# Performance work log

Hardware: AMD Instinct MI355X
Metric: run time of the kernel (lower is better)

Reference implementation:

```python
import jax, jax.numpy as jnp
import numpy as np

FEAT = 1433
HID = 2
NUM_CLASS = 7
EPS = 1e-5  # torch BatchNorm1d default eps


def _bn_softsign(h, gamma, beta):
    # BatchNorm1d in training mode: batch stats over (batch, length) per channel.
    mu = h.mean(axis=(0, 2), keepdims=True)
    var = h.var(axis=(0, 2), keepdims=True)  # biased, matches torch normalization
    hn = (h - mu) * jax.lax.rsqrt(var + EPS)
    hn = hn * gamma[None, :, None] + beta[None, :, None]
    return hn / (1.0 + jnp.abs(hn))  # Softsign


def feature_adjacency(x, y):
    # (x.unsqueeze(-1) * y.unsqueeze(-2)).sum(dim=1) with x channel dim == 1
    # reduces to an outer product of x[:,0] with neighbor.sum over K.
    adj = jnp.einsum('bf,bg->bfg', x.sum(1), y.sum(1))  # [B,F,F]
    adj = adj + jnp.swapaxes(adj, -1, -2)
    adj = jnp.sqrt(adj)
    # row_normalize: divide by sum over dim 1, zero out inf/nan
    norm = adj / adj.sum(axis=1, keepdims=True)
    norm = jnp.where(jnp.isfinite(norm), norm, 0.0)
    return norm + jnp.eye(FEAT, dtype=x.dtype)


def featbrd(x, adj, W, b):
    # adjacency-based feature conv: y[b,c,f] = sum_g adj[(b),f,g] x[b,c,g],
    # then 1x1 conv over channels (Conv1d kernel_size=1).
    if adj.shape[0] == 1:
        y = jnp.einsum('fg,bcg->bcf', adj[0], x)
    else:
        y = jnp.einsum('bfg,bcg->bcf', adj, x)
    return jnp.einsum('oc,bcf->bof', W, y) + b[None, :, None]


def setup_inputs() -> dict:
    key = jax.random.key(0)
    ks = jax.random.split(key, 10)
    B, K = 64, 8
    inp = {
        'x': jax.random.uniform(ks[0], (B, 1, FEAT), dtype=jnp.float32),
        'neighbor': jax.random.uniform(ks[1], (B, K, FEAT), dtype=jnp.float32),
        'adj_buf': jnp.zeros((1, FEAT, FEAT), jnp.float32),
        'W1': jax.random.normal(ks[2], (HID, 1), jnp.float32) * 0.5,
        'b1': jnp.zeros((HID,), jnp.float32),
        'W2': jax.random.normal(ks[3], (HID, HID), jnp.float32) * 0.5,
        'b2': jnp.zeros((HID,), jnp.float32),
        'g1': jnp.ones((HID,), jnp.float32),
        'be1': jnp.zeros((HID,), jnp.float32),
        'g2': jnp.ones((HID,), jnp.float32),
        'be2': jnp.zeros((HID,), jnp.float32),
        'Wc': jax.random.normal(ks[4], (NUM_CLASS, FEAT * HID), jnp.float32) * 0.02,
        'bc': jnp.zeros((NUM_CLASS,), jnp.float32),
    }
    return inp


def reference(x, neighbor, adj_buf, W1, b1, W2, b2, g1, be1, g2, be2, Wc, bc):
    fadj = feature_adjacency(x, neighbor)          # [B,F,F]
    adj_tot = adj_buf + fadj.sum(0)                # [1,F,F] (buffer starts at zero)
    h = _bn_softsign(featbrd(x, fadj, W1, b1), g1, be1)      # [B,HID,F]
    h = _bn_softsign(featbrd(h, adj_tot, W2, b2), g2, be2)   # [B,HID,F]
    flat = h.reshape(h.shape[0], -1)               # Flatten (C then F, row-major)
    return flat @ Wc.T + bc
```

## Files before the change

kernel.cpp:

```cpp
#include <hip/hip_runtime.h>
#include <hip/hip_bf16.h>
#include <math.h>

constexpr int F   = 1433;
constexpr int NB  = 64;
constexpr int KN  = 8;
constexpr int BF  = NB * F;
constexpr float EPS = 1e-5f;

constexpr int SF  = 16;
constexpr int CH  = 90;
constexpr int AbS = 1440;
constexpr int SK  = 15;
constexpr int FT  = 12;
constexpr int NA  = 720;
constexpr int NST = 256;

constexpr int O_YS  = 0;
constexpr int O_DP  = O_YS + BF;
constexpr int O_Y1P = O_DP + SF * BF;
constexpr int O_P   = O_Y1P + SF * BF;
constexpr int O_Y1  = O_P + 4 * BF;
constexpr int O_Y2  = O_Y1 + BF;
constexpr int O_G2P = O_Y2 + 2 * BF;
constexpr int O_AB  = O_G2P + SK * 128 * F;
constexpr int O_ST  = O_AB + (F * AbS) / 2;
constexpr int O_BAR = O_ST + 64;

__device__ __forceinline__ void devst(float* p, float v) {
  __hip_atomic_store(p, v, __ATOMIC_RELAXED, __HIP_MEMORY_SCOPE_AGENT);
}
__device__ __forceinline__ void devst16(ushort* p, ushort v) {
  __hip_atomic_store(p, v, __ATOMIC_RELAXED, __HIP_MEMORY_SCOPE_AGENT);
}
__device__ __forceinline__ void devst4(float4* p, float4 v) {
  union { float2 f; unsigned long long u; } lo, hi;
  lo.f = make_float2(v.x, v.y);
  hi.f = make_float2(v.z, v.w);
  unsigned long long* q = (unsigned long long*)p;
  __hip_atomic_store(q + 0, lo.u, __ATOMIC_RELAXED, __HIP_MEMORY_SCOPE_AGENT);
  __hip_atomic_store(q + 1, hi.u, __ATOMIC_RELAXED, __HIP_MEMORY_SCOPE_AGENT);
}
__device__ __forceinline__ float devld(const float* p) {
  return __hip_atomic_load(p, __ATOMIC_RELAXED, __HIP_MEMORY_SCOPE_AGENT);
}

__device__ __forceinline__ void grid_barrier(unsigned* bar, unsigned phase) {
  __syncthreads();
  if (threadIdx.x == 0) {
    const unsigned ngrp = gridDim.x >> 3;
    const unsigned grp = (unsigned)blockIdx.x & 7u;
    unsigned old = __hip_atomic_fetch_add(&bar[grp * 32], 1u,
                                          __ATOMIC_RELAXED, __HIP_MEMORY_SCOPE_AGENT);
    if (old == phase * ngrp - 1u) {
      unsigned m = __hip_atomic_fetch_add(&bar[256], 1u,
                                          __ATOMIC_RELAXED, __HIP_MEMORY_SCOPE_AGENT);
      if (m == phase * 8u - 1u)
        __hip_atomic_store(&bar[257], phase, __ATOMIC_RELAXED, __HIP_MEMORY_SCOPE_AGENT);
    }
    while (__hip_atomic_load(&bar[257], __ATOMIC_RELAXED, __HIP_MEMORY_SCOPE_AGENT) < phase)
      __builtin_amdgcn_s_sleep(32);
  }
  __syncthreads();
}

__global__ __launch_bounds__(256, 4) void k_fused(
    const float* __restrict__ x, const float* __restrict__ nbr,
    const float* __restrict__ W1, const float* __restrict__ g1,
    const float* __restrict__ be1, const float* __restrict__ W2,
    const float* __restrict__ b2, const float* __restrict__ g2,
    const float* __restrict__ be2, const float* __restrict__ Wc,
    const float* __restrict__ bc, float* __restrict__ out,
    float* __restrict__ ws) {
  float*  ys  = ws + O_YS;
  float*  DP  = ws + O_DP;
  float*  Y1P = ws + O_Y1P;
  float4* P   = (float4*)(ws + O_P);
  float*  y1  = ws + O_Y1;
  float*  y2  = ws + O_Y2;
  float*  G2P = ws + O_G2P;
  ushort* Ab  = (ushort*)(ws + O_AB);
  const ushort* Abu = (const ushort*)(ws + O_AB);
  float*  st  = ws + O_ST;
  unsigned* bar = (unsigned*)(ws + O_BAR);

  __shared__ __align__(16) char smem[21504];
  const int tid = threadIdx.x;
  const int gsz = (int)gridDim.x;

  {
    float2* xyc = (float2*)smem;
    for (int w = blockIdx.x; w < NB * SF; w += gsz) {
      const int b = w & 63, s = w >> 6;
      __syncthreads();
      const int cs = s * CH, cn = min(CH, F - cs);
      for (int i = tid; i < cn; i += 256) {
        const float* p = nbr + (size_t)b * KN * F + cs + i;
        float a = 0.f;
#pragma unroll
        for (int k = 0; k < KN; ++k) a += p[k * F];
        xyc[i] = make_float2(x[b * F + cs + i], a);
      }
      __syncthreads();
      float gx[6], gy[6], acc[6] = {};
#pragma unroll
      for (int j = 0; j < 6; ++j) {
        int g = tid + 256 * j;
        int gc = min(g, F - 1);
        const float* p = nbr + (size_t)b * KN * F + gc;
        float a = 0.f;
#pragma unroll
        for (int k = 0; k < KN; ++k) a += p[k * F];
        gx[j] = (g < F) ? x[b * F + gc] : 0.f;
        gy[j] = (g < F) ? a : 0.f;
      }
      if (s == 0) {
#pragma unroll
        for (int j = 0; j < 6; ++j) {
          int g = tid + 256 * j;
          if (g < F) devst(&ys[b * F + g], gy[j]);
        }
      }
#pragma unroll 6
      for (int i = 0; i < cn; ++i) {
        float2 p = xyc[i];
#pragma unroll
        for (int j = 0; j < 6; ++j)
          acc[j] += __builtin_amdgcn_sqrtf(fmaf(gy[j], p.x, gx[j] * p.y));
      }
#pragma unroll
      for (int j = 0; j < 6; ++j) {
        int g = tid + 256 * j;
        if (g < F) devst(&DP[(size_t)s * BF + b * F + g], acc[j]);
      }
    }
  }
  grid_barrier(bar, 1u);

  {
    float4* pl = (float4*)smem;
    for (int w = blockIdx.x; w < NB * SF; w += gsz) {
      const int b = w & 63, s = w >> 6;
      __syncthreads();
      const int cs = s * CH, cn = min(CH, F - cs);
      for (int i = tid; i < cn; i += 256) {
        int g = cs + i;
        float d = 0.f;
#pragma unroll
        for (int t = 0; t < SF; ++t) d += DP[(size_t)t * BF + b * F + g];
        float inv = (d > 0.f) ? 1.f / d : 0.f;
        float xv = x[b * F + g], yv = ys[b * F + g];
        float4 pv = make_float4(xv, yv, xv * inv, inv);
        pl[i] = pv;
        devst4(&P[b * F + g], pv);
      }
      __syncthreads();
      float fx[6], fys[6], acc[6] = {};
#pragma unroll
      for (int j = 0; j < 6; ++j) {
        int f = tid + 256 * j;
        fx[j]  = (f < F) ? x[b * F + f] : 0.f;
        fys[j] = (f < F) ? ys[b * F + f] : 0.f;
      }
#pragma unroll 6
      for (int i = 0; i < cn; ++i) {
        float4 p = pl[i];
#pragma unroll
        for (int j = 0; j < 6; ++j)
          acc[j] = fmaf(__builtin_amdgcn_sqrtf(fmaf(fx[j], p.y, fys[j] * p.x)), p.z, acc[j]);
      }
#pragma unroll
      for (int j = 0; j < 6; ++j) {
        int f = tid + 256 * j;
        if (f < F) devst(&Y1P[(size_t)s * BF + b * F + f], acc[j]);
      }
    }
  }
  grid_barrier(bar, 2u);

  {
    for (int w = blockIdx.x; w < NA + NST; w += gsz) {
      __syncthreads();
      if (w < NA) {
        float2 (*fxy)[NB] = (float2(*)[NB])smem;
        const int gxc = w % 6, fyt = w / 6;
        const int fbase = fyt * FT;
#pragma unroll
        for (int r = 0; r < 3; ++r) {
          int i = tid + 256 * r;
          int j = i >> 6, bb = i & 63;
          int f = fbase + j;
          float vx = 0.f, vy = 0.f;
          if (f < F) { vx = x[bb * F + f]; vy = ys[bb * F + f]; }
          fxy[j][bb] = make_float2(vx, vy);
        }
        __syncthreads();
        const int g = gxc * 256 + tid;
        if (g < F) {
          float acc[FT] = {};
          float4 cur[4], nxt[4];
#pragma unroll
          for (int t = 0; t < 4; ++t) cur[t] = P[t * F + g];
          for (int bb = 0; bb < NB; bb += 4) {
            if (bb + 4 < NB) {
#pragma unroll
              for (int t = 0; t < 4; ++t) nxt[t] = P[(bb + 4 + t) * F + g];
            }
#pragma unroll
            for (int t = 0; t < 4; ++t) {
              float4 pc = cur[t];
#pragma unroll
              for (int j = 0; j < FT; ++j) {
                float2 wv = fxy[j][bb + t];
                acc[j] = fmaf(__builtin_amdgcn_sqrtf(fmaf(wv.x, pc.y, pc.x * wv.y)), pc.w, acc[j]);
              }
            }
#pragma unroll
            for (int t = 0; t < 4; ++t) cur[t] = nxt[t];
          }
#pragma unroll
          for (int j = 0; j < FT; ++j) {
            int f = fbase + j;
            if (f < F) {
              __hip_bfloat16 hv = __float2bfloat16(acc[j]);
              devst16(&Ab[(size_t)f * AbS + g], *reinterpret_cast<ushort*>(&hv));
            }
          }
        } else if (g < AbS) {
#pragma unroll
          for (int j = 0; j < FT; ++j) {
            int f = fbase + j;
            if (f < F) devst16(&Ab[(size_t)f * AbS + g], (ushort)0);
          }
        }
      } else {
        const int sid = w - NA;
        float sv = 0.f, sq = 0.f;
        for (int i = sid * 256 + tid; i < BF; i += NST * 256) {
          float v = x[i];
#pragma unroll
          for (int t = 0; t < SF; ++t) v += Y1P[(size_t)t * BF + i];
          devst(&y1[i], v);
          sv += v; sq += v * v;
        }
#pragma unroll
        for (int o = 32; o; o >>= 1) {
          sv += __shfl_down(sv, o, 64);
          sq += __shfl_down(sq, o, 64);
        }
        float* ls = (float*)smem;
        float* lq = ls + 4;
        int wave = tid >> 6, lane = tid & 63;
        if (lane == 0) { ls[wave] = sv; lq[wave] = sq; }
        __syncthreads();
        if (tid == 0) {
          atomicAdd(&st[0], ls[0] + ls[1] + ls[2] + ls[3]);
          atomicAdd(&st[1], lq[0] + lq[1] + lq[2] + lq[3]);
        }
      }
    }
  }
  grid_barrier(bar, 3u);

  {
    const float mu  = st[0] / (float)BF;
    const float var = st[1] / (float)BF - mu * mu;
    const float wa = W1[0], wb = W1[1];
    const float k0 = wa * g1[0] / sqrtf(wa * wa * var + EPS);
    const float k1 = wb * g1[1] / sqrtf(wb * wb * var + EPS);
    const float c0 = -k0 * mu + be1[0];
    const float c1 = -k1 * mu + be1[1];

    float* Al = (float*)smem;
    float* Hl = (float*)(smem + 4608);
    const int ffs = tid >> 3, g4s = (tid & 7) * 4;
    const int hb = tid & 7, hg = tid >> 3;
    const int fsub = (tid & 7) * 4, msub = (tid >> 3) * 4;

    for (int w = blockIdx.x; w < 45 * SK; w += gsz) {
      const int fb = w % 45, sk = w / 45;
      const int f0 = fb * 32;
      const int gs = sk * 96;
      __syncthreads();

      uint2 pa; float pyv[8];
      auto loadRegs = [&](int gb) {
        const int f = f0 + ffs;
        pa = make_uint2(0u, 0u);
        if (f < F) pa = *(const uint2*)&Abu[(size_t)f * AbS + gb + g4s];
        const int gl = min(gb + hg, F - 1);
#pragma unroll
        for (int r = 0; r < 8; ++r) pyv[r] = y1[(hb + 8 * r) * F + gl];
      };
      auto storeLDS = [&]() {
        Al[(g4s + 0) * 36 + ffs] = __uint_as_float(pa.x << 16);
        Al[(g4s + 1) * 36 + ffs] = __uint_as_float(pa.x & 0xffff0000u);
        Al[(g4s + 2) * 36 + ffs] = __uint_as_float(pa.y << 16);
        Al[(g4s + 3) * 36 + ffs] = __uint_as_float(pa.y & 0xffff0000u);
#pragma unroll
        for (int r = 0; r < 8; ++r) {
          const int bb = hb + 8 * r;
          const float v = pyv[r];
          float h0 = fmaf(k0, v, c0); h0 = h0 / (1.f + fabsf(h0));
          float h1 = fmaf(k1, v, c1); h1 = h1 / (1.f + fabsf(h1));
          *(float2*)&Hl[hg * 132 + 2 * bb] = make_float2(h0, h1);
        }
      };

      float acc[4][4] = {};
      loadRegs(gs);
      for (int c = 0; c < 3; ++c) {
        if (c) __syncthreads();
        storeLDS();
        __syncthreads();
        if (c < 2) loadRegs(gs + (c + 1) * 32);
#pragma unroll 4
        for (int gi = 0; gi < 32; ++gi) {
          float4 a4 = *(const float4*)&Al[gi * 36 + fsub];
          float4 h4 = *(const float4*)&Hl[gi * 132 + msub];
          float av[4] = {a4.x, a4.y, a4.z, a4.w};
          float hv[4] = {h4.x, h4.y, h4.z, h4.w};
#pragma unroll
          for (int i = 0; i < 4; ++i)
#pragma unroll
            for (int j = 0; j < 4; ++j)
              acc[i][j] = fmaf(av[i], hv[j], acc[i][j]);
        }
      }
      float* dst = G2P + (size_t)sk * 128 * F;
#pragma unroll
      for (int i = 0; i < 4; ++i) {
        int f = f0 + fsub + i;
        if (f < F) {
#pragma unroll
          for (int j = 0; j < 4; ++j)
            devst(&dst[(msub + j) * F + f], acc[i][j]);
        }
      }
    }
  }
  grid_barrier(bar, 4u);

  {
    const float mu  = st[0] / (float)BF;
    const float var = st[1] / (float)BF - mu * mu;
    const float wa = W1[0], wb = W1[1];
    const float k0 = wa * g1[0] / sqrtf(wa * wa * var + EPS);
    const float k1 = wb * g1[1] / sqrtf(wb * wb * var + EPS);
    const float c0 = -k0 * mu + be1[0];
    const float c1 = -k1 * mu + be1[1];

    float su = 0.f, sv = 0.f, suu = 0.f, svv = 0.f, suv = 0.f;
    for (int i = blockIdx.x * 256 + tid; i < BF; i += gsz * 256) {
      int b = i / F, f = i - b * F;
      float wv = y1[i];
      float h0 = fmaf(k0, wv, c0); h0 = h0 / (1.f + fabsf(h0));
      float h1 = fmaf(k1, wv, c1); h1 = h1 / (1.f + fabsf(h1));
      int iu = (2 * b) * F + f, iv = iu + F;
      float u = 64.f * h0, v = 64.f * h1;
#pragma unroll
      for (int t = 0; t < SK; ++t) {
        u += G2P[(size_t)t * 128 * F + iu];
        v += G2P[(size_t)t * 128 * F + iv];
      }
      devst(&y2[iu], u); devst(&y2[iv], v);
      su += u; sv += v; suu += u * u; svv += v * v; suv += u * v;
    }
#pragma unroll
    for (int o = 32; o; o >>= 1) {
      su  += __shfl_down(su, o, 64);
      sv  += __shfl_down(sv, o, 64);
      suu += __shfl_down(suu, o, 64);
      svv += __shfl_down(svv, o, 64);
      suv += __shfl_down(suv, o, 64);
    }
    float (*red)[4] = (float(*)[4])smem;
    int wave = tid >> 6, lane = tid & 63;
    if (lane == 0) {
      red[0][wave] = su; red[1][wave] = sv; red[2][wave] = suu;
      red[3][wave] = svv; red[4][wave] = suv;
    }
    __syncthreads();
    if (tid == 0) {
#pragma unroll
      for (int m = 0; m < 5; ++m)
        atomicAdd(&st[2 + m], red[m][0] + red[m][1] + red[m][2] + red[m][3]);
    }
  }
  grid_barrier(bar, 5u);

  {
    float n = (float)BF;
    float Eu = devld(&st[2]) / n, Ev = devld(&st[3]) / n;
    float Euu = devld(&st[4]) / n, Evv = devld(&st[5]) / n, Euv = devld(&st[6]) / n;
    float cA[2], cB[2], cC[2];
#pragma unroll
    for (int o = 0; o < 2; ++o) {
      float w0 = W2[o * 2 + 0], w1 = W2[o * 2 + 1];
      float mean = w0 * Eu + w1 * Ev + b2[o];
      float Eh2 = w0 * w0 * Euu + 2.f * w0 * w1 * Euv + w1 * w1 * Evv +
                  2.f * b2[o] * (w0 * Eu + w1 * Ev) + b2[o] * b2[o];
      float vr = Eh2 - mean * mean;
      float inv = g2[o] / sqrtf(vr + EPS);
      cA[o] = w0 * inv;
      cB[o] = w1 * inv;
      cC[o] = (b2[o] - mean) * inv + be2[o];
    }
    float (*red)[4] = (float(*)[4])smem;
    for (int w = blockIdx.x; w < NB * 6; w += gsz) {
      const int b = w / 6, part = w % 6;
      float acc[7] = {};
      const int f = part * 256 + tid;
      if (f < F) {
        float u = y2[(2 * b) * F + f], v = y2[(2 * b + 1) * F + f];
        float h0 = fmaf(cA[0], u, fmaf(cB[0], v, cC[0]));
        h0 = h0 / (1.f + fabsf(h0));
        float h1 = fmaf(cA[1], u, fmaf(cB[1], v, cC[1]));
        h1 = h1 / (1.f + fabsf(h1));
#pragma unroll
        for (int o = 0; o < 7; ++o)
          acc[o] = fmaf(Wc[o * (2 * F) + f], h0, Wc[o * (2 * F) + F + f] * h1);
      }
#pragma unroll
      for (int o = 0; o < 7; ++o) {
#pragma unroll
        for (int s2 = 32; s2; s2 >>= 1) acc[o] += __shfl_down(acc[o], s2, 64);
      }
      __syncthreads();
      int wave = tid >> 6, lane = tid & 63;
      if (lane == 0) {
#pragma unroll
        for (int o = 0; o < 7; ++o) red[o][wave] = acc[o];
      }
      __syncthreads();
      if (tid < 7) {
        float add = red[tid][0] + red[tid][1] + red[tid][2] + red[tid][3];
        if (part == 0) add += bc[tid];
        atomicAdd(&out[b * 7 + tid], add);
      }
    }
  }
}

__global__ __launch_bounds__(256) void k_D(const float* __restrict__ x,
                                           const float* __restrict__ nbr,
                                           float* __restrict__ DP,
                                           float* __restrict__ ys_out,
                                           float* __restrict__ st) {
  const int b = blockIdx.x, s = blockIdx.y;
  if (b == 0 && s == 0 && threadIdx.x < 64) st[threadIdx.x] = 0.f;
  __shared__ __align__(8) float2 xyc[CH];
  const int cs = s * CH, cn = min(CH, F - cs);
  for (int i = threadIdx.x; i < cn; i += 256) {
    const float* p = nbr + (size_t)b * KN * F + cs + i;
    float a = 0.f;
#pragma unroll
    for (int k = 0; k < KN; ++k) a += p[k * F];
    xyc[i] = make_float2(x[b * F + cs + i], a);
  }
  __syncthreads();
  float gx[6], gy[6], acc[6] = {};
#pragma unroll
  for (int j = 0; j < 6; ++j) {
    int g = threadIdx.x + 256 * j;
    int gc = min(g, F - 1);
    const float* p = nbr + (size_t)b * KN * F + gc;
    float a = 0.f;
#pragma unroll
    for (int k = 0; k < KN; ++k) a += p[k * F];
    gx[j] = (g < F) ? x[b * F + gc] : 0.f;
    gy[j] = (g < F) ? a : 0.f;
  }
  if (s == 0) {
#pragma unroll
    for (int j = 0; j < 6; ++j) {
      int g = threadIdx.x + 256 * j;
      if (g < F) ys_out[b * F + g] = gy[j];
    }
  }
#pragma unroll 6
  for (int i = 0; i < cn; ++i) {
    float2 p = xyc[i];
#pragma unroll
    for (int j = 0; j < 6; ++j)
      acc[j] += __builtin_amdgcn_sqrtf(fmaf(gy[j], p.x, gx[j] * p.y));
  }
#pragma unroll
  for (int j = 0; j < 6; ++j) {
    int g = threadIdx.x + 256 * j;
    if (g < F) DP[(size_t)s * BF + b * F + g] = acc[j];
  }
}

__global__ __launch_bounds__(256) void k_y1(const float* __restrict__ x,
                                            const float* __restrict__ ys,
                                            const float* __restrict__ DP,
                                            float* __restrict__ Y1P,
                                            float4* __restrict__ P) {
  __shared__ __align__(16) float4 pl[CH];
  const int b = blockIdx.x, s = blockIdx.y;
  const int cs = s * CH, cn = min(CH, F - cs);
  for (int i = threadIdx.x; i < cn; i += 256) {
    int g = cs + i;
    float d = 0.f;
#pragma unroll
    for (int t = 0; t < SF; ++t) d += DP[(size_t)t * BF + b * F + g];
    float inv = (d > 0.f) ? 1.f / d : 0.f;
    float xv = x[b * F + g], yv = ys[b * F + g];
    float4 pv = make_float4(xv, yv, xv * inv, inv);
    pl[i] = pv;
    P[b * F + g] = pv;
  }
  __syncthreads();
  float fx[6], fy[6], acc[6] = {};
#pragma unroll
  for (int j = 0; j < 6; ++j) {
    int f = threadIdx.x + 256 * j;
    fx[j] = (f < F) ? x[b * F + f] : 0.f;
    fy[j] = (f < F) ? ys[b * F + f] : 0.f;
  }
#pragma unroll 6
  for (int i = 0; i < cn; ++i) {
    float4 p = pl[i];
#pragma unroll
    for (int j = 0; j < 6; ++j)
      acc[j] = fmaf(__builtin_amdgcn_sqrtf(fmaf(fx[j], p.y, fy[j] * p.x)), p.z, acc[j]);
  }
#pragma unroll
  for (int j = 0; j < 6; ++j) {
    int f = threadIdx.x + 256 * j;
    if (f < F) Y1P[(size_t)s * BF + b * F + f] = acc[j];
  }
}

__global__ __launch_bounds__(256) void k_Astats(const float* __restrict__ x,
                                                const float* __restrict__ ys,
                                                const float4* __restrict__ P,
                                                const float* __restrict__ Y1P,
                                                __hip_bfloat16* __restrict__ Ab,
                                                float* __restrict__ y1,
                                                float* __restrict__ st) {
  const int bid = blockIdx.x;
  if (bid < NA) {
    __shared__ float2 fxy[FT][NB];
    const int gxc = bid % 6, fy = bid / 6;
    const int fbase = fy * FT;
#pragma unroll
    for (int r = 0; r < 3; ++r) {
      int i = threadIdx.x + 256 * r;
      int j = i >> 6, bb = i & 63;
      int f = fbase + j;
      float vx = 0.f, vy = 0.f;
      if (f < F) { vx = x[bb * F + f]; vy = ys[bb * F + f]; }
      fxy[j][bb] = make_float2(vx, vy);
    }
    __syncthreads();
    const int g = gxc * 256 + threadIdx.x;
    if (g >= AbS) return;
    if (g < F) {
      float acc[FT] = {};
      float4 cur[4], nxt[4];
#pragma unroll
      for (int t = 0; t < 4; ++t) cur[t] = P[t * F + g];
      for (int bb = 0; bb < NB; bb += 4) {
        if (bb + 4 < NB) {
#pragma unroll
          for (int t = 0; t < 4; ++t) nxt[t] = P[(bb + 4 + t) * F + g];
        }
#pragma unroll
        for (int t = 0; t < 4; ++t) {
          float4 pc = cur[t];
#pragma unroll
          for (int j = 0; j < FT; ++j) {
            float2 w = fxy[j][bb + t];
            acc[j] = fmaf(__builtin_amdgcn_sqrtf(fmaf(w.x, pc.y, pc.x * w.y)), pc.w, acc[j]);
          }
        }
#pragma unroll
        for (int t = 0; t < 4; ++t) cur[t] = nxt[t];
      }
#pragma unroll
      for (int j = 0; j < FT; ++j) {
        int f = fbase + j;
        if (f < F) Ab[(size_t)f * AbS + g] = __float2bfloat16(acc[j]);
      }
    } else {
#pragma unroll
      for (int j = 0; j < FT; ++j) {
        int f = fbase + j;
        if (f < F) Ab[(size_t)f * AbS + g] = __float2bfloat16(0.f);
      }
    }
  } else {
    const int sid = bid - NA;
    float sv = 0.f, sq = 0.f;
    for (int i = sid * 256 + threadIdx.x; i < BF; i += NST * 256) {
      float v = x[i];
#pragma unroll
      for (int t = 0; t < SF; ++t) v += Y1P[(size_t)t * BF + i];
      y1[i] = v;
      sv += v; sq += v * v;
    }
#pragma unroll
    for (int o = 32; o; o >>= 1) {
      sv += __shfl_down(sv, o, 64);
      sq += __shfl_down(sq, o, 64);
    }
    __shared__ float ls[4], lq[4];
    int wave = threadIdx.x >> 6, lane = threadIdx.x & 63;
    if (lane == 0) { ls[wave] = sv; lq[wave] = sq; }
    __syncthreads();
    if (threadIdx.x == 0) {
      atomicAdd(&st[0], ls[0] + ls[1] + ls[2] + ls[3]);
      atomicAdd(&st[1], lq[0] + lq[1] + lq[2] + lq[3]);
    }
  }
}

__global__ __launch_bounds__(256, 4) void k_gemm(const ushort* __restrict__ Ab,
                                                 const float* __restrict__ y1,
                                                 const float* __restrict__ st,
                                                 const float* __restrict__ W1,
                                                 const float* __restrict__ g1,
                                                 const float* __restrict__ be1,
                                                 float* __restrict__ G2P) {
  const float mu = st[0] / (float)BF;
  const float var = st[1] / (float)BF - mu * mu;
  const float wa = W1[0], wb = W1[1];
  const float k0 = wa * g1[0] / sqrtf(wa * wa * var + EPS);
  const float k1 = wb * g1[1] / sqrtf(wb * wb * var + EPS);
  const float c0 = -k0 * mu + be1[0];
  const float c1 = -k1 * mu + be1[1];

  __shared__ __align__(16) float Al[32 * 36];
  __shared__ __align__(16) float Hl[32 * 132];
  const int f0 = blockIdx.x * 32;
  const int gs = blockIdx.y * 96;
  const int tid = threadIdx.x;
  const int ffs = tid >> 3, g4s = (tid & 7) * 4;
  const int hb = tid & 7, hg = tid >> 3;
  const int fsub = (tid & 7) * 4, msub = (tid >> 3) * 4;

  uint2 pa; float pyv[8];
  auto loadRegs = [&](int gb) {
    const int f = f0 + ffs;
    pa = make_uint2(0u, 0u);
    if (f < F) pa = *(const uint2*)&Ab[(size_t)f * AbS + gb + g4s];
    const int gl = min(gb + hg, F - 1);
#pragma unroll
    for (int r = 0; r < 8; ++r) pyv[r] = y1[(hb + 8 * r) * F + gl];
  };
  auto storeLDS = [&]() {
    Al[(g4s + 0) * 36 + ffs] = __uint_as_float(pa.x << 16);
    Al[(g4s + 1) * 36 + ffs] = __uint_as_float(pa.x & 0xffff0000u);
    Al[(g4s + 2) * 36 + ffs] = __uint_as_float(pa.y << 16);
    Al[(g4s + 3) * 36 + ffs] = __uint_as_float(pa.y & 0xffff0000u);
#pragma unroll
    for (int r = 0; r < 8; ++r) {
      const int bb = hb + 8 * r;
      const float v = pyv[r];
      float h0 = fmaf(k0, v, c0); h0 = h0 / (1.f + fabsf(h0));
      float h1 = fmaf(k1, v, c1); h1 = h1 / (1.f + fabsf(h1));
      *(float2*)&Hl[hg * 132 + 2 * bb] = make_float2(h0, h1);
    }
  };

  float acc[4][4] = {};
  loadRegs(gs);
  for (int c = 0; c < 3; ++c) {
    if (c) __syncthreads();
    storeLDS();
    __syncthreads();
    if (c < 2) loadRegs(gs + (c + 1) * 32);
#pragma unroll 4
    for (int gi = 0; gi < 32; ++gi) {
      float4 a4 = *(const float4*)&Al[gi * 36 + fsub];
      float4 h4 = *(const float4*)&Hl[gi * 132 + msub];
      float av[4] = {a4.x, a4.y, a4.z, a4.w};
      float hv[4] = {h4.x, h4.y, h4.z, h4.w};
#pragma unroll
      for (int i = 0; i < 4; ++i)
#pragma unroll
        for (int j = 0; j < 4; ++j)
          acc[i][j] = fmaf(av[i], hv[j], acc[i][j]);
    }
  }
  float* dst = G2P + (size_t)blockIdx.y * 128 * F;
#pragma unroll
  for (int i = 0; i < 4; ++i) {
    int f = f0 + fsub + i;
    if (f < F) {
#pragma unroll
      for (int j = 0; j < 4; ++j)
        dst[(msub + j) * F + f] = acc[i][j];
    }
  }
}

__global__ __launch_bounds__(256) void k_stats2(const float* __restrict__ y1,
                                                const float* __restrict__ G2P,
                                                const float* __restrict__ st,
                                                const float* __restrict__ W1,
                                                const float* __restrict__ g1,
                                                const float* __restrict__ be1,
                                                float* __restrict__ y2,
                                                float* __restrict__ stw) {
  const float mu = st[0] / (float)BF;
  const float var = st[1] / (float)BF - mu * mu;
  const float wa = W1[0], wb = W1[1];
  const float k0 = wa * g1[0] / sqrtf(wa * wa * var + EPS);
  const float k1 = wb * g1[1] / sqrtf(wb * wb * var + EPS);
  const float c0 = -k0 * mu + be1[0];
  const float c1 = -k1 * mu + be1[1];

  float su = 0.f, sv = 0.f, suu = 0.f, svv = 0.f, suv = 0.f;
  for (int i = blockIdx.x * 256 + threadIdx.x; i < BF; i += gridDim.x * 256) {
    int b = i / F, f = i - b * F;
    float w = y1[i];
    float h0 = fmaf(k0, w, c0); h0 = h0 / (1.f + fabsf(h0));
    float h1 = fmaf(k1, w, c1); h1 = h1 / (1.f + fabsf(h1));
    int iu = (2 * b) * F + f, iv = iu + F;
    float u = 64.f * h0, v = 64.f * h1;
#pragma unroll
    for (int t = 0; t < SK; ++t) {
      u += G2P[(size_t)t * 128 * F + iu];
      v += G2P[(size_t)t * 128 * F + iv];
    }
    y2[iu] = u; y2[iv] = v;
    su += u; sv += v; suu += u * u; svv += v * v; suv += u * v;
  }
#pragma unroll
  for (int o = 32; o; o >>= 1) {
    su += __shfl_down(su, o, 64);
    sv += __shfl_down(sv, o, 64);
    suu += __shfl_down(suu, o, 64);
    svv += __shfl_down(svv, o, 64);
    suv += __shfl_down(suv, o, 64);
  }
  __shared__ float red[5][4];
  int wave = threadIdx.x >> 6, lane = threadIdx.x & 63;
  if (lane == 0) {
    red[0][wave] = su; red[1][wave] = sv; red[2][wave] = suu;
    red[3][wave] = svv; red[4][wave] = suv;
  }
  __syncthreads();
  if (threadIdx.x == 0) {
#pragma unroll
    for (int m = 0; m < 5; ++m)
      atomicAdd(&stw[2 + m], red[m][0] + red[m][1] + red[m][2] + red[m][3]);
  }
}

__global__ __launch_bounds__(256) void k_out(const float* __restrict__ y2,
                                             const float* __restrict__ st,
                                             const float* __restrict__ W2,
                                             const float* __restrict__ b2,
                                             const float* __restrict__ g2,
                                             const float* __restrict__ be2,
                                             const float* __restrict__ Wc,
                                             const float* __restrict__ bc,
                                             float* __restrict__ out) {
  float n = (float)BF;
  float Eu = st[2] / n, Ev = st[3] / n;
  float Euu = st[4] / n, Evv = st[5] / n, Euv = st[6] / n;
  float cA[2], cB[2], cC[2];
#pragma unroll
  for (int o = 0; o < 2; ++o) {
    float w0 = W2[o * 2 + 0], w1 = W2[o * 2 + 1];
    float mean = w0 * Eu + w1 * Ev + b2[o];
    float Eh2 = w0 * w0 * Euu + 2.f * w0 * w1 * Euv + w1 * w1 * Evv +
                2.f * b2[o] * (w0 * Eu + w1 * Ev) + b2[o] * b2[o];
    float vr = Eh2 - mean * mean;
    float inv = g2[o] / sqrtf(vr + EPS);
    cA[o] = w0 * inv;
    cB[o] = w1 * inv;
    cC[o] = (b2[o] - mean) * inv + be2[o];
  }
  const int b = blockIdx.x;
  float acc[7] = {};
  for (int f = threadIdx.x; f < F; f += 256) {
    float u = y2[(2 * b) * F + f], v = y2[(2 * b + 1) * F + f];
    float h0 = fmaf(cA[0], u, fmaf(cB[0], v, cC[0]));
    h0 = h0 / (1.f + fabsf(h0));
    float h1 = fmaf(cA[1], u, fmaf(cB[1], v, cC[1]));
    h1 = h1 / (1.f + fabsf(h1));
#pragma unroll
    for (int o = 0; o < 7; ++o) acc[o] = fmaf(Wc[o * (2 * F) + f], h0, acc[o]);
#pragma unroll
    for (int o = 0; o < 7; ++o) acc[o] = fmaf(Wc[o * (2 * F) + F + f], h1, acc[o]);
  }
#pragma unroll
  for (int o = 0; o < 7; ++o) {
#pragma unroll
    for (int s = 32; s; s >>= 1) acc[o] += __shfl_down(acc[o], s, 64);
  }
  __shared__ float red[7][4];
  int wave = threadIdx.x >> 6, lane = threadIdx.x & 63;
  if (lane == 0) {
#pragma unroll
    for (int o = 0; o < 7; ++o) red[o][wave] = acc[o];
  }
  __syncthreads();
  if (threadIdx.x < 7) {
    int o = threadIdx.x;
    out[b * 7 + o] = red[o][0] + red[o][1] + red[o][2] + red[o][3] + bc[o];
  }
}

extern "C" void kernel_launch(void* const* d_in, const int* in_sizes, int n_in,
                              void* d_out, int out_size, void* d_ws, size_t ws_size,
                              hipStream_t stream) {
  const float* x    = (const float*)d_in[0];
  const float* nbr  = (const float*)d_in[1];
  const float* W1   = (const float*)d_in[3];
  const float* W2   = (const float*)d_in[5];
  const float* b2   = (const float*)d_in[6];
  const float* g1   = (const float*)d_in[7];
  const float* be1  = (const float*)d_in[8];
  const float* g2   = (const float*)d_in[9];
  const float* be2  = (const float*)d_in[10];
  const float* Wc   = (const float*)d_in[11];
  const float* bc   = (const float*)d_in[12];
  float* out = (float*)d_out;
  float* ws  = (float*)d_ws;

  float*  ys  = ws + O_YS;
  float*  DP  = ws + O_DP;
  float*  Y1P = ws + O_Y1P;
  float4* P   = (float4*)(ws + O_P);
  float*  y1  = ws + O_Y1;
  float*  y2  = ws + O_Y2;
  float*  G2P = ws + O_G2P;
  __hip_bfloat16* Ab = (__hip_bfloat16*)(ws + O_AB);
  float*  st  = ws + O_ST;

  static int nblk = -1;
  if (nblk < 0) {
    int dev = 0;
    (void)hipGetDevice(&dev);
    int cus = 0;
    if (hipDeviceGetAttribute(&cus, hipDeviceAttributeMultiprocessorCount, dev) != hipSuccess || cus <= 0)
      cus = 256;
    int nb = 0;
    if (hipOccupancyMaxActiveBlocksPerMultiprocessor(
            &nb, reinterpret_cast<const void*>(&k_fused), 256, 0) != hipSuccess)
      nb = 0;
    long cap = (long)nb * (long)cus;
    long want = (cap >= 1024) ? 1024 : (cap / 8) * 8;
    nblk = (int)want;
  }

  if (nblk >= 256) {
    hipMemsetAsync((void*)(ws + O_ST), 0, 2048, stream);
    hipMemsetAsync(d_out, 0, (size_t)out_size, stream);
    k_fused<<<dim3(nblk), dim3(256), 0, stream>>>(x, nbr, W1, g1, be1, W2, b2,
                                                  g2, be2, Wc, bc, out, ws);
  } else {
    k_D     <<<dim3(NB, SF), 256, 0, stream>>>(x, nbr, DP, ys, st);
    k_y1    <<<dim3(NB, SF), 256, 0, stream>>>(x, ys, DP, Y1P, P);
    k_Astats<<<NA + NST, 256, 0, stream>>>(x, ys, P, Y1P, Ab, y1, st);
    k_gemm  <<<dim3(45, SK), 256, 0, stream>>>((const ushort*)Ab, y1, st, W1, g1, be1, G2P);
    k_stats2<<<NST, 256, 0, stream>>>(y1, G2P, st, W1, g1, be1, y2, st);
    k_out   <<<NB, 256, 0, stream>>>(y2, st, W2, b2, g2, be2, Wc, bc, out);
  }
}
```

Measured before the change: 236.2 us.

## Add separate neighbor-sum phase, retile phases for more resident blocks

Adds a dedicated first phase that computes the neighbor sum ys once and publishes it behind an extra grid barrier, so later phases read it instead of recomputing eight-row sums redundantly. Splits work finer (SF 28, CH 52, FT 6) and raises occupancy target to 7 blocks per CU with a grid of up to 1792 blocks to use more CUs. The final classifier now has one block per sample writing output directly, removing the output memset and atomics. Costs an additional grid-wide barrier, and more partial sums to reduce in the second phase, and register pressure from the higher occupancy bound.

```diff
diff --git a/kernel.cpp b/kernel.cpp
--- a/kernel.cpp
+++ b/kernel.cpp
@@ -8,13 +8,15 @@
 constexpr int BF  = NB * F;
 constexpr float EPS = 1e-5f;
 
-constexpr int SF  = 16;
-constexpr int CH  = 90;
+constexpr int SF  = 28;
+constexpr int CH  = 52;
 constexpr int AbS = 1440;
 constexpr int SK  = 15;
-constexpr int FT  = 12;
-constexpr int NA  = 720;
+constexpr int FT  = 6;
+constexpr int NFT = 239;
+constexpr int NA  = NFT * 6;
 constexpr int NST = 256;
+constexpr int NGRID = 1792;
 
 constexpr int O_YS  = 0;
 constexpr int O_DP  = O_YS + BF;
@@ -59,12 +61,12 @@
         __hip_atomic_store(&bar[257], phase, __ATOMIC_RELAXED, __HIP_MEMORY_SCOPE_AGENT);
     }
     while (__hip_atomic_load(&bar[257], __ATOMIC_RELAXED, __HIP_MEMORY_SCOPE_AGENT) < phase)
-      __builtin_amdgcn_s_sleep(32);
+      __builtin_amdgcn_s_sleep(16);
   }
   __syncthreads();
 }
 
-__global__ __launch_bounds__(256, 4) void k_fused(
+__global__ __launch_bounds__(256, 7) void k_fused(
     const float* __restrict__ x, const float* __restrict__ nbr,
     const float* __restrict__ W1, const float* __restrict__ g1,
     const float* __restrict__ be1, const float* __restrict__ W2,
@@ -88,40 +90,37 @@
   const int tid = threadIdx.x;
   const int gsz = (int)gridDim.x;
 
+  for (int w = blockIdx.x; w < NB * SF; w += gsz) {
+    const int b = w & 63, s = w >> 6;
+    const int cs = s * CH, cn = min(CH, F - cs);
+    if (tid < cn) {
+      const float* p = nbr + (size_t)b * KN * F + cs + tid;
+      float a = 0.f;
+#pragma unroll
+      for (int k = 0; k < KN; ++k) a += p[k * F];
+      devst(&ys[b * F + cs + tid], a);
+    }
+  }
+  grid_barrier(bar, 1u);
+
   {
     float2* xyc = (float2*)smem;
     for (int w = blockIdx.x; w < NB * SF; w += gsz) {
       const int b = w & 63, s = w >> 6;
       __syncthreads();
       const int cs = s * CH, cn = min(CH, F - cs);
-      for (int i = tid; i < cn; i += 256) {
-        const float* p = nbr + (size_t)b * KN * F + cs + i;
-        float a = 0.f;
-#pragma unroll
-        for (int k = 0; k < KN; ++k) a += p[k * F];
-        xyc[i] = make_float2(x[b * F + cs + i], a);
-      }
+      if (tid < cn)
+        xyc[tid] = make_float2(x[b * F + cs + tid], ys[b * F + cs + tid]);
       __syncthreads();
       float gx[6], gy[6], acc[6] = {};
 #pragma unroll
       for (int j = 0; j < 6; ++j) {
         int g = tid + 256 * j;
         int gc = min(g, F - 1);
-        const float* p = nbr + (size_t)b * KN * F + gc;
-        float a = 0.f;
-#pragma unroll
-        for (int k = 0; k < KN; ++k) a += p[k * F];
         gx[j] = (g < F) ? x[b * F + gc] : 0.f;
-        gy[j] = (g < F) ? a : 0.f;
-      }
-      if (s == 0) {
-#pragma unroll
-        for (int j = 0; j < 6; ++j) {
-          int g = tid + 256 * j;
-          if (g < F) devst(&ys[b * F + g], gy[j]);
-        }
-      }
-#pragma unroll 6
+        gy[j] = (g < F) ? ys[b * F + gc] : 0.f;
+      }
+#pragma unroll 4
       for (int i = 0; i < cn; ++i) {
         float2 p = xyc[i];
 #pragma unroll
@@ -135,7 +134,7 @@
       }
     }
   }
-  grid_barrier(bar, 1u);
+  grid_barrier(bar, 2u);
 
   {
     float4* pl = (float4*)smem;
@@ -143,15 +142,15 @@
       const int b = w & 63, s = w >> 6;
       __syncthreads();
       const int cs = s * CH, cn = min(CH, F - cs);
-      for (int i = tid; i < cn; i += 256) {
-        int g = cs + i;
+      if (tid < cn) {
+        int g = cs + tid;
         float d = 0.f;
 #pragma unroll
         for (int t = 0; t < SF; ++t) d += DP[(size_t)t * BF + b * F + g];
         float inv = (d > 0.f) ? 1.f / d : 0.f;
         float xv = x[b * F + g], yv = ys[b * F + g];
         float4 pv = make_float4(xv, yv, xv * inv, inv);
-        pl[i] = pv;
+        pl[tid] = pv;
         devst4(&P[b * F + g], pv);
       }
       __syncthreads();
@@ -159,10 +158,11 @@
 #pragma unroll
       for (int j = 0; j < 6; ++j) {
         int f = tid + 256 * j;
-        fx[j]  = (f < F) ? x[b * F + f] : 0.f;
-        fys[j] = (f < F) ? ys[b * F + f] : 0.f;
-      }
-#pragma unroll 6
+        int fc = min(f, F - 1);
+        fx[j]  = (f < F) ? x[b * F + fc] : 0.f;
+        fys[j] = (f < F) ? ys[b * F + fc] : 0.f;
+      }
+#pragma unroll 4
       for (int i = 0; i < cn; ++i) {
         float4 p = pl[i];
 #pragma unroll
@@ -176,7 +176,7 @@
       }
     }
   }
-  grid_barrier(bar, 2u);
+  grid_barrier(bar, 3u);
 
   {
     for (int w = blockIdx.x; w < NA + NST; w += gsz) {
@@ -186,13 +186,15 @@
         const int gxc = w % 6, fyt = w / 6;
         const int fbase = fyt * FT;
 #pragma unroll
-        for (int r = 0; r < 3; ++r) {
+        for (int r = 0; r < 2; ++r) {
           int i = tid + 256 * r;
-          int j = i >> 6, bb = i & 63;
-          int f = fbase + j;
-          float vx = 0.f, vy = 0.f;
-          if (f < F) { vx = x[bb * F + f]; vy = ys[bb * F + f]; }
-          fxy[j][bb] = make_float2(vx, vy);
+          if (i < FT * NB) {
+            int j = i >> 6, bb = i & 63;
+            int f = fbase + j;
+            float vx = 0.f, vy = 0.f;
+            if (f < F) { vx = x[bb * F + f]; vy = ys[bb * F + f]; }
+            fxy[j][bb] = make_float2(vx, vy);
+          }
         }
         __syncthreads();
         const int g = gxc * 256 + tid;
@@ -260,7 +262,7 @@
       }
     }
   }
-  grid_barrier(bar, 3u);
+  grid_barrier(bar, 4u);
 
   {
     const float mu  = st[0] / (float)BF;
@@ -339,7 +341,7 @@
       }
     }
   }
-  grid_barrier(bar, 4u);
+  grid_barrier(bar, 5u);
 
   {
     const float mu  = st[0] / (float)BF;
@@ -387,7 +389,7 @@
         atomicAdd(&st[2 + m], red[m][0] + red[m][1] + red[m][2] + red[m][3]);
     }
   }
-  grid_barrier(bar, 5u);
+  grid_barrier(bar, 6u);
 
   {
     float n = (float)BF;
@@ -407,11 +409,10 @@
       cC[o] = (b2[o] - mean) * inv + be2[o];
     }
     float (*red)[4] = (float(*)[4])smem;
-    for (int w = blockIdx.x; w < NB * 6; w += gsz) {
-      const int b = w / 6, part = w % 6;
+    for (int w = blockIdx.x; w < NB; w += gsz) {
+      const int b = w;
       float acc[7] = {};
-      const int f = part * 256 + tid;
-      if (f < F) {
+      for (int f = tid; f < F; f += 256) {
         float u = y2[(2 * b) * F + f], v = y2[(2 * b + 1) * F + f];
         float h0 = fmaf(cA[0], u, fmaf(cB[0], v, cC[0]));
         h0 = h0 / (1.f + fabsf(h0));
@@ -419,7 +420,8 @@
         h1 = h1 / (1.f + fabsf(h1));
 #pragma unroll
         for (int o = 0; o < 7; ++o)
-          acc[o] = fmaf(Wc[o * (2 * F) + f], h0, Wc[o * (2 * F) + F + f] * h1);
+          acc[o] = fmaf(Wc[o * (2 * F) + f], h0,
+                        fmaf(Wc[o * (2 * F) + F + f], h1, acc[o]));
       }
 #pragma unroll
       for (int o = 0; o < 7; ++o) {
@@ -433,11 +435,9 @@
         for (int o = 0; o < 7; ++o) red[o][wave] = acc[o];
       }
       __syncthreads();
-      if (tid < 7) {
-        float add = red[tid][0] + red[tid][1] + red[tid][2] + red[tid][3];
-        if (part == 0) add += bc[tid];
-        atomicAdd(&out[b * 7 + tid], add);
-      }
+      if (tid < 7)
+        out[b * 7 + tid] =
+            red[tid][0] + red[tid][1] + red[tid][2] + red[tid][3] + bc[tid];
     }
   }
 }
@@ -478,7 +478,7 @@
       if (g < F) ys_out[b * F + g] = gy[j];
     }
   }
-#pragma unroll 6
+#pragma unroll 4
   for (int i = 0; i < cn; ++i) {
     float2 p = xyc[i];
 #pragma unroll
@@ -519,7 +519,7 @@
     fx[j] = (f < F) ? x[b * F + f] : 0.f;
     fy[j] = (f < F) ? ys[b * F + f] : 0.f;
   }
-#pragma unroll 6
+#pragma unroll 4
   for (int i = 0; i < cn; ++i) {
     float4 p = pl[i];
 #pragma unroll
@@ -546,13 +546,15 @@
     const int gxc = bid % 6, fy = bid / 6;
     const int fbase = fy * FT;
 #pragma unroll
-    for (int r = 0; r < 3; ++r) {
+    for (int r = 0; r < 2; ++r) {
       int i = threadIdx.x + 256 * r;
-      int j = i >> 6, bb = i & 63;
-      int f = fbase + j;
-      float vx = 0.f, vy = 0.f;
-      if (f < F) { vx = x[bb * F + f]; vy = ys[bb * F + f]; }
-      fxy[j][bb] = make_float2(vx, vy);
+      if (i < FT * NB) {
+        int j = i >> 6, bb = i & 63;
+        int f = fbase + j;
+        float vx = 0.f, vy = 0.f;
+        if (f < F) { vx = x[bb * F + f]; vy = ys[bb * F + f]; }
+        fxy[j][bb] = make_float2(vx, vy);
+      }
     }
     __syncthreads();
     const int g = gxc * 256 + threadIdx.x;
@@ -846,13 +848,12 @@
             &nb, reinterpret_cast<const void*>(&k_fused), 256, 0) != hipSuccess)
       nb = 0;
     long cap = (long)nb * (long)cus;
-    long want = (cap >= 1024) ? 1024 : (cap / 8) * 8;
+    long want = (cap >= NGRID) ? NGRID : (cap / 8) * 8;
     nblk = (int)want;
   }
 
   if (nblk >= 256) {
     hipMemsetAsync((void*)(ws + O_ST), 0, 2048, stream);
-    hipMemsetAsync(d_out, 0, (size_t)out_size, stream);
     k_fused<<<dim3(nblk), dim3(256), 0, stream>>>(x, nbr, W1, g1, be1, W2, b2,
                                                   g2, be2, Wc, bc, out, ws);
   } else {
```

After: 264.7 us. 12.1% more time.

## Double fused kernel block size to 512 threads and rebalance all phases

Applied to the files above, without the earlier changes.

The persistent fused kernel now runs with 512-thread blocks instead of 256. Every phase's work split is rewritten to match: half the per-thread column registers in the first two phases, three column groups instead of six in the A build, paired 32-row tiles per block in the GEMM, and 8-wave reductions. The output phase now gives each batch row to a single block and writes the result directly, which removes the output memset and the atomics. The aim is fewer, larger work items with lower grid-barrier and scheduling overhead, at the cost of heavier per-block register and LDS pressure and a possible change in occupancy.

```diff
diff --git a/kernel.cpp b/kernel.cpp
--- a/kernel.cpp
+++ b/kernel.cpp
@@ -13,8 +13,13 @@
 constexpr int AbS = 1440;
 constexpr int SK  = 15;
 constexpr int FT  = 12;
-constexpr int NA  = 720;
+constexpr int NFT = 120;
+constexpr int NAF = NFT * 3;
+constexpr int NAL = NFT * 6;
 constexpr int NST = 256;
+constexpr int NFP = 23;
+constexpr int NGU = NFP * SK;
+constexpr int NGRID = 1024;
 
 constexpr int O_YS  = 0;
 constexpr int O_DP  = O_YS + BF;
@@ -64,7 +69,7 @@
   __syncthreads();
 }
 
-__global__ __launch_bounds__(256, 4) void k_fused(
+__global__ __launch_bounds__(512, 8) void k_fused(
     const float* __restrict__ x, const float* __restrict__ nbr,
     const float* __restrict__ W1, const float* __restrict__ g1,
     const float* __restrict__ be1, const float* __restrict__ W2,
@@ -84,7 +89,7 @@
   float*  st  = ws + O_ST;
   unsigned* bar = (unsigned*)(ws + O_BAR);
 
-  __shared__ __align__(16) char smem[21504];
+  __shared__ __align__(16) char smem[26112];
   const int tid = threadIdx.x;
   const int gsz = (int)gridDim.x;
 
@@ -94,18 +99,18 @@
       const int b = w & 63, s = w >> 6;
       __syncthreads();
       const int cs = s * CH, cn = min(CH, F - cs);
-      for (int i = tid; i < cn; i += 256) {
-        const float* p = nbr + (size_t)b * KN * F + cs + i;
+      if (tid < cn) {
+        const float* p = nbr + (size_t)b * KN * F + cs + tid;
         float a = 0.f;
 #pragma unroll
         for (int k = 0; k < KN; ++k) a += p[k * F];
-        xyc[i] = make_float2(x[b * F + cs + i], a);
+        xyc[tid] = make_float2(x[b * F + cs + tid], a);
       }
       __syncthreads();
-      float gx[6], gy[6], acc[6] = {};
-#pragma unroll
-      for (int j = 0; j < 6; ++j) {
-        int g = tid + 256 * j;
+      float gx[3], gy[3], acc[3] = {};
+#pragma unroll
+      for (int j = 0; j < 3; ++j) {
+        int g = tid + 512 * j;
         int gc = min(g, F - 1);
         const float* p = nbr + (size_t)b * KN * F + gc;
         float a = 0.f;
@@ -116,8 +121,8 @@
       }
       if (s == 0) {
 #pragma unroll
-        for (int j = 0; j < 6; ++j) {
-          int g = tid + 256 * j;
+        for (int j = 0; j < 3; ++j) {
+          int g = tid + 512 * j;
           if (g < F) devst(&ys[b * F + g], gy[j]);
         }
       }
@@ -125,12 +130,12 @@
       for (int i = 0; i < cn; ++i) {
         float2 p = xyc[i];
 #pragma unroll
-        for (int j = 0; j < 6; ++j)
+        for (int j = 0; j < 3; ++j)
           acc[j] += __builtin_amdgcn_sqrtf(fmaf(gy[j], p.x, gx[j] * p.y));
       }
 #pragma unroll
-      for (int j = 0; j < 6; ++j) {
-        int g = tid + 256 * j;
+      for (int j = 0; j < 3; ++j) {
+        int g = tid + 512 * j;
         if (g < F) devst(&DP[(size_t)s * BF + b * F + g], acc[j]);
       }
     }
@@ -143,35 +148,36 @@
       const int b = w & 63, s = w >> 6;
       __syncthreads();
       const int cs = s * CH, cn = min(CH, F - cs);
-      for (int i = tid; i < cn; i += 256) {
-        int g = cs + i;
+      if (tid < cn) {
+        int g = cs + tid;
         float d = 0.f;
 #pragma unroll
         for (int t = 0; t < SF; ++t) d += DP[(size_t)t * BF + b * F + g];
         float inv = (d > 0.f) ? 1.f / d : 0.f;
         float xv = x[b * F + g], yv = ys[b * F + g];
         float4 pv = make_float4(xv, yv, xv * inv, inv);
-        pl[i] = pv;
+        pl[tid] = pv;
         devst4(&P[b * F + g], pv);
       }
       __syncthreads();
-      float fx[6], fys[6], acc[6] = {};
-#pragma unroll
-      for (int j = 0; j < 6; ++j) {
-        int f = tid + 256 * j;
-        fx[j]  = (f < F) ? x[b * F + f] : 0.f;
-        fys[j] = (f < F) ? ys[b * F + f] : 0.f;
+      float fx[3], fys[3], acc[3] = {};
+#pragma unroll
+      for (int j = 0; j < 3; ++j) {
+        int f = tid + 512 * j;
+        int fc = min(f, F - 1);
+        fx[j]  = (f < F) ? x[b * F + fc] : 0.f;
+        fys[j] = (f < F) ? ys[b * F + fc] : 0.f;
       }
 #pragma unroll 6
       for (int i = 0; i < cn; ++i) {
         float4 p = pl[i];
 #pragma unroll
-        for (int j = 0; j < 6; ++j)
+        for (int j = 0; j < 3; ++j)
           acc[j] = fmaf(__builtin_amdgcn_sqrtf(fmaf(fx[j], p.y, fys[j] * p.x)), p.z, acc[j]);
       }
 #pragma unroll
-      for (int j = 0; j < 6; ++j) {
-        int f = tid + 256 * j;
+      for (int j = 0; j < 3; ++j) {
+        int f = tid + 512 * j;
         if (f < F) devst(&Y1P[(size_t)s * BF + b * F + f], acc[j]);
       }
     }
@@ -179,23 +185,25 @@
   grid_barrier(bar, 2u);
 
   {
-    for (int w = blockIdx.x; w < NA + NST; w += gsz) {
+    for (int w = blockIdx.x; w < NAF + NST; w += gsz) {
       __syncthreads();
-      if (w < NA) {
+      if (w < NAF) {
         float2 (*fxy)[NB] = (float2(*)[NB])smem;
-        const int gxc = w % 6, fyt = w / 6;
+        const int gxc = w % 3, fyt = w / 3;
         const int fbase = fyt * FT;
 #pragma unroll
-        for (int r = 0; r < 3; ++r) {
-          int i = tid + 256 * r;
-          int j = i >> 6, bb = i & 63;
-          int f = fbase + j;
-          float vx = 0.f, vy = 0.f;
-          if (f < F) { vx = x[bb * F + f]; vy = ys[bb * F + f]; }
-          fxy[j][bb] = make_float2(vx, vy);
+        for (int r = 0; r < 2; ++r) {
+          int i = tid + 512 * r;
+          if (i < FT * NB) {
+            int j = i >> 6, bb = i & 63;
+            int f = fbase + j;
+            float vx = 0.f, vy = 0.f;
+            if (f < F) { vx = x[bb * F + f]; vy = ys[bb * F + f]; }
+            fxy[j][bb] = make_float2(vx, vy);
+          }
         }
         __syncthreads();
-        const int g = gxc * 256 + tid;
+        const int g = gxc * 512 + tid;
         if (g < F) {
           float acc[FT] = {};
           float4 cur[4], nxt[4];
@@ -234,9 +242,9 @@
           }
         }
       } else {
-        const int sid = w - NA;
+        const int sid = w - NAF;
         float sv = 0.f, sq = 0.f;
-        for (int i = sid * 256 + tid; i < BF; i += NST * 256) {
+        for (int i = sid * 512 + tid; i < BF; i += NST * 512) {
           float v = x[i];
 #pragma unroll
           for (int t = 0; t < SF; ++t) v += Y1P[(size_t)t * BF + i];
@@ -249,13 +257,16 @@
           sq += __shfl_down(sq, o, 64);
         }
         float* ls = (float*)smem;
-        float* lq = ls + 4;
+        float* lq = ls + 8;
         int wave = tid >> 6, lane = tid & 63;
         if (lane == 0) { ls[wave] = sv; lq[wave] = sq; }
         __syncthreads();
         if (tid == 0) {
-          atomicAdd(&st[0], ls[0] + ls[1] + ls[2] + ls[3]);
-          atomicAdd(&st[1], lq[0] + lq[1] + lq[2] + lq[3]);
+          float a = 0.f, bsum = 0.f;
+#pragma unroll
+          for (int q = 0; q < 8; ++q) { a += ls[q]; bsum += lq[q]; }
+          atomicAdd(&st[0], a);
+          atomicAdd(&st[1], bsum);
         }
       }
     }
@@ -271,15 +282,16 @@
     const float c0 = -k0 * mu + be1[0];
     const float c1 = -k1 * mu + be1[1];
 
-    float* Al = (float*)smem;
-    float* Hl = (float*)(smem + 4608);
-    const int ffs = tid >> 3, g4s = (tid & 7) * 4;
-    const int hb = tid & 7, hg = tid >> 3;
-    const int fsub = (tid & 7) * 4, msub = (tid >> 3) * 4;
-
-    for (int w = blockIdx.x; w < 45 * SK; w += gsz) {
-      const int fb = w % 45, sk = w / 45;
-      const int f0 = fb * 32;
+    const int half = tid >> 8, t = tid & 255;
+    float* Al = (float*)smem + half * (32 * 36);
+    float* Hl = (float*)smem + 2 * (32 * 36);
+    const int ffs = t >> 3, g4s = (t & 7) * 4;
+    const int hb = t & 7, hg = t >> 3;
+    const int fsub = (t & 7) * 4, msub = (t >> 3) * 4;
+
+    for (int w = blockIdx.x; w < NGU; w += gsz) {
+      const int fp = w % NFP, sk = w / NFP;
+      const int f0 = fp * 64 + half * 32;
       const int gs = sk * 96;
       __syncthreads();
 
@@ -351,7 +363,7 @@
     const float c1 = -k1 * mu + be1[1];
 
     float su = 0.f, sv = 0.f, suu = 0.f, svv = 0.f, suv = 0.f;
-    for (int i = blockIdx.x * 256 + tid; i < BF; i += gsz * 256) {
+    for (int i = blockIdx.x * 512 + tid; i < BF; i += gsz * 512) {
       int b = i / F, f = i - b * F;
       float wv = y1[i];
       float h0 = fmaf(k0, wv, c0); h0 = h0 / (1.f + fabsf(h0));
@@ -374,7 +386,7 @@
       svv += __shfl_down(svv, o, 64);
       suv += __shfl_down(suv, o, 64);
     }
-    float (*red)[4] = (float(*)[4])smem;
+    float (*red)[8] = (float(*)[8])smem;
     int wave = tid >> 6, lane = tid & 63;
     if (lane == 0) {
       red[0][wave] = su; red[1][wave] = sv; red[2][wave] = suu;
@@ -383,8 +395,12 @@
     __syncthreads();
     if (tid == 0) {
 #pragma unroll
-      for (int m = 0; m < 5; ++m)
-        atomicAdd(&st[2 + m], red[m][0] + red[m][1] + red[m][2] + red[m][3]);
+      for (int m = 0; m < 5; ++m) {
+        float a = 0.f;
+#pragma unroll
+        for (int q = 0; q < 8; ++q) a += red[m][q];
+        atomicAdd(&st[2 + m], a);
+      }
     }
   }
   grid_barrier(bar, 5u);
@@ -406,12 +422,11 @@
       cB[o] = w1 * inv;
       cC[o] = (b2[o] - mean) * inv + be2[o];
     }
-    float (*red)[4] = (float(*)[4])smem;
-    for (int w = blockIdx.x; w < NB * 6; w += gsz) {
-      const int b = w / 6, part = w % 6;
+    float (*red)[8] = (float(*)[8])smem;
+    for (int w = blockIdx.x; w < NB; w += gsz) {
+      const int b = w;
       float acc[7] = {};
-      const int f = part * 256 + tid;
-      if (f < F) {
+      for (int f = tid; f < F; f += 512) {
         float u = y2[(2 * b) * F + f], v = y2[(2 * b + 1) * F + f];
         float h0 = fmaf(cA[0], u, fmaf(cB[0], v, cC[0]));
         h0 = h0 / (1.f + fabsf(h0));
@@ -419,7 +434,8 @@
         h1 = h1 / (1.f + fabsf(h1));
 #pragma unroll
         for (int o = 0; o < 7; ++o)
-          acc[o] = fmaf(Wc[o * (2 * F) + f], h0, Wc[o * (2 * F) + F + f] * h1);
+          acc[o] = fmaf(Wc[o * (2 * F) + f], h0,
+                        fmaf(Wc[o * (2 * F) + F + f], h1, acc[o]));
       }
 #pragma unroll
       for (int o = 0; o < 7; ++o) {
@@ -434,9 +450,10 @@
       }
       __syncthreads();
       if (tid < 7) {
-        float add = red[tid][0] + red[tid][1] + red[tid][2] + red[tid][3];
-        if (part == 0) add += bc[tid];
-        atomicAdd(&out[b * 7 + tid], add);
+        float a = bc[tid];
+#pragma unroll
+        for (int q = 0; q < 8; ++q) a += red[tid][q];
+        out[b * 7 + tid] = a;
       }
     }
   }
@@ -541,7 +558,7 @@
                                                 float* __restrict__ y1,
                                                 float* __restrict__ st) {
   const int bid = blockIdx.x;
-  if (bid < NA) {
+  if (bid < NAL) {
     __shared__ float2 fxy[FT][NB];
     const int gxc = bid % 6, fy = bid / 6;
     const int fbase = fy * FT;
@@ -592,7 +609,7 @@
       }
     }
   } else {
-    const int sid = bid - NA;
+    const int sid = bid - NAL;
     float sv = 0.f, sq = 0.f;
     for (int i = sid * 256 + threadIdx.x; i < BF; i += NST * 256) {
       float v = x[i];
@@ -843,22 +860,21 @@
       cus = 256;
     int nb = 0;
     if (hipOccupancyMaxActiveBlocksPerMultiprocessor(
-            &nb, reinterpret_cast<const void*>(&k_fused), 256, 0) != hipSuccess)
+            &nb, reinterpret_cast<const void*>(&k_fused), 512, 0) != hipSuccess)
       nb = 0;
     long cap = (long)nb * (long)cus;
-    long want = (cap >= 1024) ? 1024 : (cap / 8) * 8;
+    long want = (cap >= NGRID) ? NGRID : (cap / 8) * 8;
     nblk = (int)want;
   }
 
   if (nblk >= 256) {
     hipMemsetAsync((void*)(ws + O_ST), 0, 2048, stream);
-    hipMemsetAsync(d_out, 0, (size_t)out_size, stream);
-    k_fused<<<dim3(nblk), dim3(256), 0, stream>>>(x, nbr, W1, g1, be1, W2, b2,
+    k_fused<<<dim3(nblk), dim3(512), 0, stream>>>(x, nbr, W1, g1, be1, W2, b2,
                                                   g2, be2, Wc, bc, out, ws);
   } else {
     k_D     <<<dim3(NB, SF), 256, 0, stream>>>(x, nbr, DP, ys, st);
     k_y1    <<<dim3(NB, SF), 256, 0, stream>>>(x, ys, DP, Y1P, P);
-    k_Astats<<<NA + NST, 256, 0, stream>>>(x, ys, P, Y1P, Ab, y1, st);
+    k_Astats<<<NAL + NST, 256, 0, stream>>>(x, ys, P, Y1P, Ab, y1, st);
     k_gemm  <<<dim3(45, SK), 256, 0, stream>>>((const ushort*)Ab, y1, st, W1, g1, be1, G2P);
     k_stats2<<<NST, 256, 0, stream>>>(y1, G2P, st, W1, g1, be1, y2, st);
     k_out   <<<NB, 256, 0, stream>>>(y2, st, W2, b2, g2, be2, Wc, bc, out);
```

Measured after the change: 269.0 us. 1.14x slower.
